# Kernel optimization log

Measured on AMD Instinct MI355X. Metric: run time of the kernel, lower is better.

## Reference

```python
import jax, jax.numpy as jnp
import numpy as np

B, N, C, H = 16384, 7, 512, 256  # batch, nodes(=n_classes), graph_hidden, hidden_layers
EPS = 1e-5


def bn(x, g, b):
    # training-mode BatchNorm1d over channels: stats over (batch, nodes)
    m = x.mean(axis=(0, 1))
    v = x.var(axis=(0, 1))  # biased variance, matches torch training BN
    return (x - m) * jax.lax.rsqrt(v + EPS) * g + b


def gcr(x, Wq, bq, Wk, bk, Wv, bv, gam):
    # GraphContextReasoning: SAGAN-style self-attention over the N node axis
    q = x @ Wq.T + bq            # [B, N, C/8]
    k = x @ Wk.T + bk            # [B, N, C/8]
    v = x @ Wv.T + bv            # [B, N, C]
    att = jax.nn.softmax(jnp.einsum('bnd,bmd->bnm', q, k), axis=-1)  # [B, N, N]
    return gam * jnp.einsum('bnm,bmc->bnc', att, v) + x


def setup_inputs() -> dict:
    ks = jax.random.split(jax.random.key(0), 40)
    it = iter(range(40))
    def rnd(shape, s=0.05):
        return jax.random.normal(ks[next(it)], shape, jnp.float32) * s
    d = {"x": jax.random.normal(ks[next(it)], (B, N, C), jnp.float32)}
    d["Wt"], d["bt"] = rnd((C, C)), rnd((C,))
    for i in ("1", "2", "3"):
        d["bn" + i + "_g"] = jnp.ones((C,), jnp.float32)
        d["bn" + i + "_b"] = jnp.zeros((C,), jnp.float32)
        d["Wq" + i], d["bq" + i] = rnd((C // 8, C)), rnd((C // 8,))
        d["Wk" + i], d["bk" + i] = rnd((C // 8, C)), rnd((C // 8,))
        d["Wv" + i], d["bv" + i] = rnd((C, C)), rnd((C,))
        d["gam" + i] = jnp.array(0.5, jnp.float32)  # torch inits 0; nonzero for nontrivial math
    d["Wb"], d["bb"] = rnd((H, C)), rnd((H,))
    return d


def reference(x, Wt, bt,
              bn1_g, bn1_b, Wq1, bq1, Wk1, bk1, Wv1, bv1, gam1,
              bn2_g, bn2_b, Wq2, bq2, Wk2, bk2, Wv2, bv2, gam2,
              bn3_g, bn3_b, Wq3, bq3, Wk3, bk3, Wv3, bv3, gam3,
              Wb, bb):
    # conv1x1 over channels == per-node linear; we keep (B, N, C) layout throughout
    h = x @ Wt.T + bt
    h = jax.nn.relu(gcr(bn(h, bn1_g, bn1_b), Wq1, bq1, Wk1, bk1, Wv1, bv1, gam1))
    h = jax.nn.relu(gcr(bn(h, bn2_g, bn2_b), Wq2, bq2, Wk2, bk2, Wv2, bv2, gam2))
    h = jax.nn.relu(gcr(bn(h, bn3_g, bn3_b), Wq3, bq3, Wk3, bk3, Wv3, bv3, gam3))
    return h @ Wb.T + bb  # [B, N, H]
```

## Files before the change

kernel.cpp:

```cpp
#include <hip/hip_runtime.h>
#include <hip/hip_bf16.h>
#include <stdint.h>


using bf16 = __hip_bfloat16;
typedef __attribute__((ext_vector_type(8))) short short8;
typedef __attribute__((ext_vector_type(4))) float f32x4;
typedef _Float16 f16x8 __attribute__((ext_vector_type(8)));

__device__ inline uint16_t f2b_bits(float f) {
  bf16 h = __float2bfloat16(f);
  return __builtin_bit_cast(uint16_t, h);
}
__device__ inline float b2f_bits(uint16_t u) { return __uint_as_float(((uint32_t)u) << 16); }
__device__ inline void split2(float v, uint16_t& hi, uint16_t& lo) {
  hi = f2b_bits(v);
  lo = f2b_bits(v - b2f_bits(hi));
}
__device__ inline uint16_t f2h_bits(float f) {
  _Float16 h = (_Float16)f;
  return __builtin_bit_cast(uint16_t, h);
}
__device__ inline float h2f_bits(uint16_t u) {
  return (float)__builtin_bit_cast(_Float16, u);
}
__device__ inline float g16(const uint4& u, int e) {
  uint32_t wrd = ((const uint32_t*)&u)[e >> 1];
  return h2f_bits((uint16_t)((e & 1) ? (wrd >> 16) : (wrd & 0xffffu)));
}

typedef const __attribute__((address_space(1))) void* gas_ptr;
typedef __attribute__((address_space(3))) void* las_ptr;
__device__ inline void gload16(const void* g, void* l) {
  __builtin_amdgcn_global_load_lds((gas_ptr)g, (las_ptr)l, 16, 0, 0);
}

__global__ __launch_bounds__(256) void cvt4h(const float* __restrict__ in,
                                             uint16_t* __restrict__ out, int n4) {
  int i = blockIdx.x * 256 + threadIdx.x;
  const int stride = gridDim.x * 256;
  for (; i < n4; i += stride) {
    float4 v = ((const float4*)in)[i];
    uint32_t lo = (uint32_t)f2h_bits(v.x) | ((uint32_t)f2h_bits(v.y) << 16);
    uint32_t hi = (uint32_t)f2h_bits(v.z) | ((uint32_t)f2h_bits(v.w) << 16);
    ((uint2*)out)[i] = make_uint2(lo, hi);
  }
}

__global__ __launch_bounds__(512) void fold_w_io(const float* __restrict__ Wsrc,
                                                 const float* __restrict__ bsrc,
                                                 char* __restrict__ Wio,
                                                 float* __restrict__ bout) {
  const int row = blockIdx.x, c = threadIdx.x;
  const float wv = Wsrc[(size_t)row * 512 + c];
  uint16_t hb, lb;
  split2(wv, hb, lb);
  char* p = Wio + (size_t)row * 2048 + (c >> 3) * 32 + (c & 7) * 2;
  *(uint16_t*)p = hb;
  *(uint16_t*)(p + 16) = lb;
  if (c == 0) bout[row] = bsrc[row];
}

__global__ __launch_bounds__(512) void fold_all(const float* __restrict__ Wq,
                                                const float* __restrict__ bq,
                                                const float* __restrict__ Wk,
                                                const float* __restrict__ bk,
                                                const float* __restrict__ Wv,
                                                const float* __restrict__ bv,
                                                const float* __restrict__ sv,
                                                const float* __restrict__ tv,
                                                const float* __restrict__ gamp,
                                                uint16_t* __restrict__ WqkH,
                                                uint16_t* __restrict__ WqkL,
                                                float* __restrict__ bqkf,
                                                uint16_t* __restrict__ WvH,
                                                float* __restrict__ bvf) {
  const int b = blockIdx.x, c = threadIdx.x;
  __shared__ float red[512];
  const float* Wsrc;
  const float* bsrc;
  uint16_t *Wh, *Wl;
  float* bout;
  float g;
  int row;
  if (b < 64) {
    Wsrc = Wq; bsrc = bq; Wh = WqkH; Wl = WqkL; bout = bqkf; g = 1.0f; row = b;
  } else if (b < 128) {
    Wsrc = Wk; bsrc = bk; Wh = WqkH + (size_t)64 * 512; Wl = WqkL + (size_t)64 * 512;
    bout = bqkf + 64; g = 1.0f; row = b - 64;
  } else {
    Wsrc = Wv; bsrc = bv; Wh = WvH; Wl = nullptr; bout = bvf; g = gamp[0]; row = b - 128;
  }
  const float wv = Wsrc[(size_t)row * 512 + c];
  const float fv = g * wv * sv[c];
  const uint16_t hb = f2h_bits(fv);
  Wh[(size_t)row * 512 + c] = hb;
  if (Wl) Wl[(size_t)row * 512 + c] = f2h_bits((fv - h2f_bits(hb)) * 1024.0f);
  red[c] = wv * tv[c];
  __syncthreads();
#pragma unroll
  for (int off = 256; off > 0; off >>= 1) {
    if (c < off) red[c] += red[c + off];
    __syncthreads();
  }
  if (c == 0) bout[row] = g * (bsrc[row] + red[0]);
}

__global__ __launch_bounds__(512, 1) void gemm1(const char* __restrict__ A,
                                                const char* __restrict__ Wio,
                                                const float* __restrict__ bias,
                                                uint16_t* __restrict__ outh,
                                                float* __restrict__ part) {
  constexpr int A_BYTES = 224 * 128;
  constexpr int PER_BUF = A_BYTES + 256 * 128;
  __shared__ __align__(16) char lds[2 * PER_BUF];
  __shared__ float sred[2][2][256];
  const int tid = threadIdx.x, w = tid >> 6, l = tid & 63;

  const int nwgx = gridDim.x;
  const int raw = blockIdx.y * nwgx + blockIdx.x;
  const int cpx = (nwgx * gridDim.y) >> 3;
  const int work = (raw & 7) * cpx + (raw >> 3);
  const int bmidx = work / nwgx;
  const int bm = bmidx * 224;
  const int bn = (work % nwgx) * 256;

  const int ssl = ((((l >> 1) & 3) ^ ((l >> 3) & 3)) << 5) | (((l & 1) ^ ((l >> 5) & 1)) << 4);
  const char* Asrc = A + (size_t)(bm + (l >> 3)) * 2048 + ssl;
  const char* Bsrc = Wio + (size_t)(bn + (l >> 3)) * 2048 + ssl;

  const int lrow = l & 15, lk = l >> 4;
  const int wr = w >> 2, wc = w & 3;
  const int sw32 = (lk ^ (lrow & 3)) * 32;
  const int hi16 = ((lrow >> 2) & 1) * 16;
  const int afr = (wr * 112 + lrow) * 128 + sw32;
  const int bfr = A_BYTES + (wc * 64 + lrow) * 128 + sw32;

  f32x4 acc[7][4] = {};

  auto stage_a = [&](int buf, int t) {
    char* dst = lds + buf * PER_BUF;
    const char* src = Asrc + (size_t)t * 128;
#pragma unroll
    for (int k = 0; k < 4; ++k) {
      const int i = w + k * 8;
      if (k < 3 || w < 4) gload16(src + (size_t)i * 16384, dst + i * 1024);
    }
  };
  auto stage_b = [&](int buf, int t) {
    char* dst = lds + buf * PER_BUF + A_BYTES;
    const char* src = Bsrc + (size_t)t * 128;
#pragma unroll
    for (int k = 0; k < 4; ++k) {
      const int i = w + k * 8;
      gload16(src + (size_t)i * 16384, dst + i * 1024);
    }
  };

#define LOADA(BASE, CNT)                                                         \
  {                                                                              \
    _Pragma("unroll") for (int u = 0; u < (CNT); ++u) {                          \
      const int mi = (BASE) + u;                                                 \
      float4 f0 = *(const float4*)(bp + afr + mi * 2048 + hi16);                 \
      float4 f1 = *(const float4*)(bp + afr + mi * 2048 + (hi16 ^ 16));          \
      const float fv[8] = {f0.x, f0.y, f0.z, f0.w, f1.x, f1.y, f1.z, f1.w};      \
      _Pragma("unroll") for (int e = 0; e < 8; ++e) {                            \
        uint16_t hb, lb;                                                         \
        split2(fv[e], hb, lb);                                                   \
        ah[u][e] = (short)hb;                                                    \
        al[u][e] = (short)lb;                                                    \
      }                                                                          \
    }                                                                            \
  }

#define MFMAC(BASE, CNT)                                                         \
  {                                                                              \
    __builtin_amdgcn_s_setprio(1);                                               \
    _Pragma("unroll") for (int u = 0; u < (CNT); ++u)                            \
      _Pragma("unroll") for (int ni = 0; ni < 4; ++ni)                           \
        acc[(BASE) + u][ni] = __builtin_amdgcn_mfma_f32_16x16x32_bf16(           \
            ah[u], bh[ni], acc[(BASE) + u][ni], 0, 0, 0);                        \
    _Pragma("unroll") for (int u = 0; u < (CNT); ++u)                            \
      _Pragma("unroll") for (int ni = 0; ni < 4; ++ni)                           \
        acc[(BASE) + u][ni] = __builtin_amdgcn_mfma_f32_16x16x32_bf16(           \
            ah[u], bl[ni], acc[(BASE) + u][ni], 0, 0, 0);                        \
    _Pragma("unroll") for (int u = 0; u < (CNT); ++u)                            \
      _Pragma("unroll") for (int ni = 0; ni < 4; ++ni)                           \
        acc[(BASE) + u][ni] = __builtin_amdgcn_mfma_f32_16x16x32_bf16(           \
            al[u], bh[ni], acc[(BASE) + u][ni], 0, 0, 0);                        \
    __builtin_amdgcn_s_setprio(0);                                               \
  }

  stage_a(0, 0);
  stage_b(0, 0);
  int cur = 0;
#pragma unroll 2
  for (int t = 0; t < 16; ++t) {
    asm volatile("s_waitcnt vmcnt(0)" ::: "memory");
    __builtin_amdgcn_s_barrier();
    asm volatile("" ::: "memory");

    const char* bp = lds + cur * PER_BUF;
    if (t < 15) stage_a(cur ^ 1, t + 1);

    short8 bh[4], bl[4];
#pragma unroll
    for (int ni = 0; ni < 4; ++ni) {
      bh[ni] = *(const short8*)(bp + bfr + ni * 2048 + hi16);
      bl[ni] = *(const short8*)(bp + bfr + ni * 2048 + (hi16 ^ 16));
    }
    short8 ah[4], al[4];
    LOADA(0, 4)
    MFMAC(0, 4)
    if (t < 15) stage_b(cur ^ 1, t + 1);
    LOADA(4, 3)
    MFMAC(4, 3)
    cur ^= 1;
  }
#undef LOADA
#undef MFMAC

  float sni[4] = {}, qni[4] = {};
#pragma unroll
  for (int mi = 0; mi < 7; ++mi) {
    const int row = bm + wr * 112 + mi * 16 + lk * 4;
#pragma unroll
    for (int ni = 0; ni < 4; ++ni) {
      const int col = bn + wc * 64 + ni * 16 + lrow;
      const float bc = bias[col];
#pragma unroll
      for (int j = 0; j < 4; ++j) {
        const float vv = acc[mi][ni][j] + bc;
        outh[(size_t)(row + j) * 512 + col] = f2h_bits(vv);
        sni[ni] += vv;
        qni[ni] += vv * vv;
      }
    }
  }
#pragma unroll
  for (int ni = 0; ni < 4; ++ni) {
    float s = sni[ni], q = qni[ni];
    s += __shfl_xor(s, 16); q += __shfl_xor(q, 16);
    s += __shfl_xor(s, 32); q += __shfl_xor(q, 32);
    if (lk == 0) {
      sred[0][wr][wc * 64 + ni * 16 + lrow] = s;
      sred[1][wr][wc * 64 + ni * 16 + lrow] = q;
    }
  }
  __syncthreads();
  if (tid < 256) {
    part[(size_t)bmidx * 1024 + bn + tid] = sred[0][0][tid] + sred[0][1][tid];
    part[(size_t)bmidx * 1024 + 512 + bn + tid] = sred[1][0][tid] + sred[1][1][tid];
  }
}

__global__ __launch_bounds__(512, 1) void sgemmV(const uint16_t* __restrict__ A,
                                                 const uint16_t* __restrict__ Wh,
                                                 const float* __restrict__ bias,
                                                 uint16_t* __restrict__ outh) {
  constexpr int A_BYTES = 112 * 128;
  constexpr int B_BYTES = 512 * 128;
  constexpr int PER_BUF = A_BYTES + B_BYTES;
  __shared__ __align__(16) char lds[2 * PER_BUF];
  const int tid = threadIdx.x, w = tid >> 6, l = tid & 63;

  const int raw = blockIdx.y;
  const int cpx = gridDim.y >> 3;
  const int bmidx = (raw & 7) * cpx + (raw >> 3);
  const int bm = bmidx * 112;

  const int sp = (((l & 7) ^ ((l >> 3) & 7)) << 4);
  const char* Asrc = (const char*)A + (size_t)(bm + (l >> 3)) * 1024 + sp;
  const char* Bhs = (const char*)Wh + (size_t)(l >> 3) * 1024 + sp;

  const int lrow = l & 15, lk = l >> 4;

  f32x4 acc[7][4] = {};

  auto stage_a = [&](int buf, int t) {
    char* dst = lds + buf * PER_BUF;
    const char* src = Asrc + t * 128;
#pragma unroll
    for (int k = 0; k < 2; ++k) {
      const int i = w + k * 8;
      if (k < 1 || w < 6) gload16(src + (size_t)i * 8192, dst + i * 1024);
    }
  };
  auto stage_b = [&](int buf, int t) {
    char* dst = lds + buf * PER_BUF + A_BYTES;
#pragma unroll
    for (int k = 0; k < 8; ++k) {
      const int i = w + k * 8;
      gload16(Bhs + t * 128 + (size_t)i * 8192, dst + i * 1024);
    }
  };

#define AFR(mi, kc) \
  (((mi)*16 + lrow) * 128 + ((((kc)*4 + lk) ^ (lrow & 7)) << 4))
#define BFR(ni, kc) \
  (A_BYTES + (w * 64 + (ni)*16 + lrow) * 128 + ((((kc)*4 + lk) ^ (lrow & 7)) << 4))

#define KHALF(kc)                                                                \
  {                                                                              \
    short8 bh[4];                                                                \
    _Pragma("unroll") for (int ni = 0; ni < 4; ++ni)                             \
        bh[ni] = *(const short8*)(bp + BFR(ni, kc));                             \
    short8 ah[7];                                                                \
    _Pragma("unroll") for (int mi = 0; mi < 7; ++mi)                             \
        ah[mi] = *(const short8*)(bp + AFR(mi, kc));                             \
    __builtin_amdgcn_s_setprio(1);                                               \
    _Pragma("unroll") for (int mi = 0; mi < 7; ++mi)                             \
      _Pragma("unroll") for (int ni = 0; ni < 4; ++ni)                           \
        acc[mi][ni] = __builtin_amdgcn_mfma_f32_16x16x32_f16(                    \
            __builtin_bit_cast(f16x8, ah[mi]), __builtin_bit_cast(f16x8, bh[ni]), \
            acc[mi][ni], 0, 0, 0);                                               \
    __builtin_amdgcn_s_setprio(0);                                               \
  }

  stage_a(0, 0);
  stage_b(0, 0);
  int cur = 0;
  for (int t = 0; t < 8; ++t) {
    asm volatile("s_waitcnt vmcnt(0)" ::: "memory");
    __builtin_amdgcn_s_barrier();
    asm volatile("" ::: "memory");
    const char* bp = lds + cur * PER_BUF;
    if (t < 7) stage_a(cur ^ 1, t + 1);
    KHALF(0)
    if (t < 7) stage_b(cur ^ 1, t + 1);
    KHALF(1)
    cur ^= 1;
  }
#undef KHALF
#undef AFR
#undef BFR

#pragma unroll
  for (int mi = 0; mi < 7; ++mi) {
    const int row = bm + mi * 16 + lk * 4;
#pragma unroll
    for (int ni = 0; ni < 4; ++ni) {
      const int col = w * 64 + ni * 16 + lrow;
      const float bc = bias[col];
#pragma unroll
      for (int j = 0; j < 4; ++j)
        outh[(size_t)(row + j) * 512 + col] = f2h_bits(acc[mi][ni][j] + bc);
    }
  }
}

__global__ __launch_bounds__(512, 1) void sgemm64(const uint16_t* __restrict__ A,
                                                  const uint16_t* __restrict__ Wh,
                                                  const float* __restrict__ bias,
                                                  float* __restrict__ outf, int N) {
  constexpr int BN = 256;
  constexpr int NFR = BN / 64;
  constexpr int A_BYTES = 224 * 128;
  constexpr int PER_BUF = A_BYTES + BN * 128;
  __shared__ __align__(16) char lds[2 * PER_BUF];
  const int tid = threadIdx.x, w = tid >> 6, l = tid & 63;

  const int nwgx = gridDim.x;
  const int raw = blockIdx.y * nwgx + blockIdx.x;
  const int cpx = (nwgx * gridDim.y) >> 3;
  const int work = (raw & 7) * cpx + (raw >> 3);
  const int bmidx = work / nwgx;
  const int bm = bmidx * 224;
  const int bn = (work % nwgx) * BN;

  const int sp = (((l & 7) ^ ((l >> 3) & 7)) << 4);
  const char* Asrc = (const char*)A + (size_t)(bm + (l >> 3)) * 1024 + sp;
  const char* Bhs = (const char*)Wh + (size_t)(bn + (l >> 3)) * 1024 + sp;

  const int lrow = l & 15, lk = l >> 4;
  const int wr = w >> 2, wc = w & 3;

  f32x4 acc[7][NFR] = {};

  auto stage_a = [&](int buf, int t) {
    char* dst = lds + buf * PER_BUF;
    const char* src = Asrc + t * 128;
#pragma unroll
    for (int k = 0; k < 4; ++k) {
      const int i = w + k * 8;
      if (k < 3 || w < 4) gload16(src + (size_t)i * 8192, dst + i * 1024);
    }
  };
  auto stage_b = [&](int buf, int t) {
    char* dst = lds + buf * PER_BUF + A_BYTES;
#pragma unroll
    for (int k = 0; k < BN / 64; ++k) {
      const int i = w + k * 8;
      gload16(Bhs + t * 128 + (size_t)i * 8192, dst + i * 1024);
    }
  };

#define AFR(mi, kc) \
  ((wr * 112 + (mi)*16 + lrow) * 128 + ((((kc)*4 + lk) ^ (lrow & 7)) << 4))
#define BFR(ni, kc) \
  (A_BYTES + (wc * (BN / 4) + (ni)*16 + lrow) * 128 + ((((kc)*4 + lk) ^ (lrow & 7)) << 4))

#define KHALF(kc)                                                                \
  {                                                                              \
    short8 bh[NFR];                                                              \
    _Pragma("unroll") for (int ni = 0; ni < NFR; ++ni)                           \
        bh[ni] = *(const short8*)(bp + BFR(ni, kc));                             \
    short8 ah[7];                                                                \
    _Pragma("unroll") for (int mi = 0; mi < 7; ++mi)                             \
        ah[mi] = *(const short8*)(bp + AFR(mi, kc));                             \
    __builtin_amdgcn_s_setprio(1);                                               \
    _Pragma("unroll") for (int mi = 0; mi < 7; ++mi)                             \
      _Pragma("unroll") for (int ni = 0; ni < NFR; ++ni)                         \
        acc[mi][ni] = __builtin_amdgcn_mfma_f32_16x16x32_f16(                    \
            __builtin_bit_cast(f16x8, ah[mi]), __builtin_bit_cast(f16x8, bh[ni]), \
            acc[mi][ni], 0, 0, 0);                                               \
    __builtin_amdgcn_s_setprio(0);                                               \
  }

  stage_a(0, 0);
  stage_b(0, 0);
  int cur = 0;
  for (int t = 0; t < 8; ++t) {
    asm volatile("s_waitcnt vmcnt(0)" ::: "memory");
    __builtin_amdgcn_s_barrier();
    asm volatile("" ::: "memory");
    const char* bp = lds + cur * PER_BUF;
    if (t < 7) stage_a(cur ^ 1, t + 1);
    KHALF(0)
    if (t < 7) stage_b(cur ^ 1, t + 1);
    KHALF(1)
    cur ^= 1;
  }
#undef KHALF
#undef AFR
#undef BFR

#pragma unroll
  for (int mi = 0; mi < 7; ++mi) {
    const int row = bm + wr * 112 + mi * 16 + lk * 4;
#pragma unroll
    for (int ni = 0; ni < NFR; ++ni) {
      const int col = bn + wc * (BN / 4) + ni * 16 + lrow;
      const float bc = bias[col];
#pragma unroll
      for (int j = 0; j < 4; ++j)
        outf[(size_t)(row + j) * N + col] = acc[mi][ni][j] + bc;
    }
  }
}

template <bool STATS>
__global__ __launch_bounds__(512, 1) void qkattn(const uint16_t* __restrict__ A,
                                                 const uint16_t* __restrict__ Wh,
                                                 const uint16_t* __restrict__ Wl,
                                                 const float* __restrict__ bias,
                                                 const uint16_t* __restrict__ V,
                                                 uint16_t* __restrict__ Hs,
                                                 const float* __restrict__ sv,
                                                 const float* __restrict__ tv,
                                                 float* __restrict__ part) {
  constexpr int A_BYTES = 224 * 128;
  constexpr int BPL = 128 * 128;
  constexpr int PER_BUF = A_BYTES + 2 * BPL;
  __shared__ __align__(16) char lds[131072];
  const int tid = threadIdx.x, w = tid >> 6, l = tid & 63;

  const int raw = blockIdx.y;
  const int cpx = gridDim.y >> 3;
  const int bmidx = (raw & 7) * cpx + (raw >> 3);
  const int bm = bmidx * 224;

  const int sp = (((l & 7) ^ ((l >> 3) & 7)) << 4);
  const char* Asrc = (const char*)A + (size_t)(bm + (l >> 3)) * 1024 + sp;
  const char* Bhs = (const char*)Wh + (size_t)(l >> 3) * 1024 + sp;
  const char* Bls = (const char*)Wl + (size_t)(l >> 3) * 1024 + sp;

  const int lrow = l & 15, lk = l >> 4;
  const int wr = w >> 2, wc = w & 3;

  f32x4 acc[7][2] = {};
  f32x4 acc2[7][2] = {};

  auto stage_a = [&](int buf, int t) {
    char* dst = lds + buf * PER_BUF;
    const char* src = Asrc + t * 128;
#pragma unroll
    for (int k = 0; k < 4; ++k) {
      const int i = w + k * 8;
      if (k < 3 || w < 4) gload16(src + (size_t)i * 8192, dst + i * 1024);
    }
  };
  auto stage_b = [&](int buf, int t) {
    char* dst = lds + buf * PER_BUF + A_BYTES;
#pragma unroll
    for (int k = 0; k < 2; ++k) {
      const int i = w + k * 8;
      gload16(Bhs + t * 128 + (size_t)i * 8192, dst + i * 1024);
      gload16(Bls + t * 128 + (size_t)i * 8192, dst + BPL + i * 1024);
    }
  };

#define AFR(mi, kc) \
  ((wr * 112 + (mi)*16 + lrow) * 128 + ((((kc)*4 + lk) ^ (lrow & 7)) << 4))
#define BFR(ni, kc) \
  (A_BYTES + (wc * 32 + (ni)*16 + lrow) * 128 + ((((kc)*4 + lk) ^ (lrow & 7)) << 4))

#define KHALF(kc)                                                                \
  {                                                                              \
    short8 bh[2], bl2[2];                                                        \
    _Pragma("unroll") for (int ni = 0; ni < 2; ++ni) {                           \
      bh[ni] = *(const short8*)(bp + BFR(ni, kc));                               \
      bl2[ni] = *(const short8*)(bp + BPL + BFR(ni, kc));                        \
    }                                                                            \
    short8 ah[7];                                                                \
    _Pragma("unroll") for (int mi = 0; mi < 7; ++mi)                             \
        ah[mi] = *(const short8*)(bp + AFR(mi, kc));                             \
    __builtin_amdgcn_s_setprio(1);                                               \
    _Pragma("unroll") for (int mi = 0; mi < 7; ++mi)                             \
      _Pragma("unroll") for (int ni = 0; ni < 2; ++ni)                           \
        acc[mi][ni] = __builtin_amdgcn_mfma_f32_16x16x32_f16(                    \
            __builtin_bit_cast(f16x8, ah[mi]), __builtin_bit_cast(f16x8, bh[ni]), \
            acc[mi][ni], 0, 0, 0);                                               \
    _Pragma("unroll") for (int mi = 0; mi < 7; ++mi)                             \
      _Pragma("unroll") for (int ni = 0; ni < 2; ++ni)                           \
        acc2[mi][ni] = __builtin_amdgcn_mfma_f32_16x16x32_f16(                   \
            __builtin_bit_cast(f16x8, ah[mi]), __builtin_bit_cast(f16x8, bl2[ni]), \
            acc2[mi][ni], 0, 0, 0);                                              \
    __builtin_amdgcn_s_setprio(0);                                               \
  }

  stage_a(0, 0);
  stage_b(0, 0);
  int cur = 0;
  for (int t = 0; t < 8; ++t) {
    asm volatile("s_waitcnt vmcnt(0)" ::: "memory");
    __builtin_amdgcn_s_barrier();
    asm volatile("" ::: "memory");
    const char* bp = lds + cur * PER_BUF;
    if (t < 7) stage_a(cur ^ 1, t + 1);
    KHALF(0)
    if (t < 7) stage_b(cur ^ 1, t + 1);
    KHALF(1)
    cur ^= 1;
  }
#undef KHALF
#undef AFR
#undef BFR

  __syncthreads();
  float* qk = (float*)lds;
#pragma unroll
  for (int mi = 0; mi < 7; ++mi) {
    const int rl = wr * 112 + mi * 16 + lk * 4;
#pragma unroll
    for (int ni = 0; ni < 2; ++ni) {
      const int col = wc * 32 + ni * 16 + lrow;
      const float bc = bias[col];
#pragma unroll
      for (int j = 0; j < 4; ++j)
        qk[(rl + j) * 128 + col] = acc[mi][ni][j] + bc + acc2[mi][ni][j] * (1.0f / 1024.0f);
    }
  }
  __syncthreads();

  const float4 s0 = *(const float4*)&sv[l * 8], s1 = *(const float4*)&sv[l * 8 + 4];
  const float4 t0 = *(const float4*)&tv[l * 8], t1 = *(const float4*)&tv[l * 8 + 4];
  const float sarr[8] = {s0.x, s0.y, s0.z, s0.w, s1.x, s1.y, s1.z, s1.w};
  const float tarr[8] = {t0.x, t0.y, t0.z, t0.w, t1.x, t1.y, t1.z, t1.w};

  float s8[8] = {}, q8[8] = {};
#pragma unroll
  for (int gg = 0; gg < 4; ++gg) {
    const int g = w * 4 + gg;
    const int rl = g * 7;
    const size_t base = (size_t)bm + rl;

    float qv[7], kv[7];
#pragma unroll
    for (int i = 0; i < 7; ++i) {
      qv[i] = qk[(rl + i) * 128 + l];
      kv[i] = qk[(rl + i) * 128 + 64 + l];
    }
    float att[7][7];
#pragma unroll
    for (int i = 0; i < 7; ++i)
#pragma unroll
      for (int j = 0; j < 7; ++j) {
        float p = qv[i] * kv[j];
#pragma unroll
        for (int o = 32; o; o >>= 1) p += __shfl_xor(p, o);
        att[i][j] = p;
      }
#pragma unroll
    for (int i = 0; i < 7; ++i) {
      float m = att[i][0];
#pragma unroll
      for (int j = 1; j < 7; ++j) m = fmaxf(m, att[i][j]);
      float sum = 0.f;
#pragma unroll
      for (int j = 0; j < 7; ++j) {
        att[i][j] = expf(att[i][j] - m);
        sum += att[i][j];
      }
      const float inv = 1.0f / sum;
#pragma unroll
      for (int j = 0; j < 7; ++j) att[i][j] *= inv;
    }

    uint4 vpk[7];
#pragma unroll
    for (int j = 0; j < 7; ++j)
      vpk[j] = *(const uint4*)((const char*)V + (base + j) * 1024 + l * 16);

#pragma unroll
    for (int i = 0; i < 7; ++i) {
      char* hp = (char*)Hs + (base + i) * 1024 + l * 16;
      uint4 hh = *(const uint4*)hp;
      float o[8] = {};
#pragma unroll
      for (int j = 0; j < 7; ++j) {
        const float a = att[i][j];
#pragma unroll
        for (int e = 0; e < 8; ++e) o[e] += a * g16(vpk[j], e);
      }
      uint16_t oh[8];
#pragma unroll
      for (int e = 0; e < 8; ++e) {
        const float xn = g16(hh, e) * sarr[e] + tarr[e];
        const float rr = fmaxf(o[e] + xn, 0.f);
        if constexpr (STATS) { s8[e] += rr; q8[e] += rr * rr; }
        oh[e] = f2h_bits(rr);
      }
      uint4 ph;
#pragma unroll
      for (int k2 = 0; k2 < 4; ++k2)
        ((uint32_t*)&ph)[k2] = (uint32_t)oh[2 * k2] | ((uint32_t)oh[2 * k2 + 1] << 16);
      *(uint4*)hp = ph;
    }
  }

  if constexpr (STATS) {
    float* sred = (float*)(lds + 114688);
#pragma unroll
    for (int e = 0; e < 8; ++e) sred[w * 512 + l * 8 + e] = s8[e];
    __syncthreads();
    {
      float sum = 0.f;
#pragma unroll
      for (int ww = 0; ww < 8; ++ww) sum += sred[ww * 512 + tid];
      part[(size_t)bmidx * 1024 + tid] = sum;
    }
    __syncthreads();
#pragma unroll
    for (int e = 0; e < 8; ++e) sred[w * 512 + l * 8 + e] = q8[e];
    __syncthreads();
    {
      float sum = 0.f;
#pragma unroll
      for (int ww = 0; ww < 8; ++ww) sum += sred[ww * 512 + tid];
      part[(size_t)bmidx * 1024 + 512 + tid] = sum;
    }
  }
}

__global__ __launch_bounds__(64) void reduce_stats(const float* __restrict__ part, int n,
                                                   const float* __restrict__ g,
                                                   const float* __restrict__ bb,
                                                   float* __restrict__ sv,
                                                   float* __restrict__ tv) {
  const int c = blockIdx.x, k = threadIdx.x;
  float sum = 0.f, sq = 0.f;
  for (int i = k; i < n; i += 64) {
    const float* p = part + (size_t)i * 1024;
    sum += p[c];
    sq += p[512 + c];
  }
#pragma unroll
  for (int o = 32; o; o >>= 1) {
    sum += __shfl_xor(sum, o);
    sq += __shfl_xor(sq, o);
  }
  if (k == 0) {
    const float mean = sum * (1.0f / 114688.0f);
    const float var = sq * (1.0f / 114688.0f) - mean * mean;
    const float sc = g[c] * rsqrtf(var + 1e-5f);
    sv[c] = sc;
    tv[c] = bb[c] - mean * sc;
  }
}

extern "C" void kernel_launch(void* const* d_in, const int* in_sizes, int n_in,
                              void* d_out, int out_size, void* d_ws, size_t ws_size,
                              hipStream_t stream) {
  const float* x  = (const float*)d_in[0];
  const float* Wt = (const float*)d_in[1];
  const float* bt = (const float*)d_in[2];
  const float *bng[3], *bnb[3], *Wq[3], *bq[3], *Wk[3], *bk[3], *Wv[3], *bv[3], *gam[3];
  for (int i = 0; i < 3; ++i) {
    int o = 3 + 9 * i;
    bng[i] = (const float*)d_in[o + 0];
    bnb[i] = (const float*)d_in[o + 1];
    Wq[i]  = (const float*)d_in[o + 2];
    bq[i]  = (const float*)d_in[o + 3];
    Wk[i]  = (const float*)d_in[o + 4];
    bk[i]  = (const float*)d_in[o + 5];
    Wv[i]  = (const float*)d_in[o + 6];
    bv[i]  = (const float*)d_in[o + 7];
    gam[i] = (const float*)d_in[o + 8];
  }
  const float* Wb = (const float*)d_in[30];
  const float* bb = (const float*)d_in[31];

  char* ws = (char*)d_ws;
  uint16_t* Hs    = (uint16_t*)(ws);
  uint16_t* V     = (uint16_t*)(ws + 117440512);
  float*    part  = (float*)(ws + 234881024);
  float*    sv    = (float*)(ws + 236978176);
  float*    tv    = (float*)(ws + 236980224);
  uint16_t* WqkH  = (uint16_t*)(ws + 236982272);
  uint16_t* WqkL  = (uint16_t*)(ws + 237113344);
  float*    bqkf  = (float*)(ws + 237244416);
  uint16_t* WvH   = (uint16_t*)(ws + 237246464);
  float*    bvf   = (float*)(ws + 237770752);
  char*     WtIo  = ws + 237772800;
  float*    btf   = (float*)(ws + 238821376);
  uint16_t* WbH   = (uint16_t*)(ws + 238823424);

  cvt4h<<<128, 256, 0, stream>>>(Wb, WbH, 32768);
  fold_w_io<<<512, 512, 0, stream>>>(Wt, bt, WtIo, btf);

  gemm1<<<dim3(2, 512), 512, 0, stream>>>((const char*)x, WtIo, btf, Hs, part);

  for (int i = 0; i < 3; ++i) {
    reduce_stats<<<512, 64, 0, stream>>>(part, 512, bng[i], bnb[i], sv, tv);
    fold_all<<<640, 512, 0, stream>>>(Wq[i], bq[i], Wk[i], bk[i], Wv[i], bv[i],
                                      sv, tv, gam[i], WqkH, WqkL, bqkf, WvH, bvf);
    sgemmV<<<dim3(1, 1024), 512, 0, stream>>>(Hs, WvH, bvf, V);
    if (i < 2)
      qkattn<true><<<dim3(1, 512), 512, 0, stream>>>(Hs, WqkH, WqkL, bqkf, V, Hs,
                                                     sv, tv, part);
    else
      qkattn<false><<<dim3(1, 512), 512, 0, stream>>>(Hs, WqkH, WqkL, bqkf, V, Hs,
                                                      sv, tv, nullptr);
  }

  sgemm64<<<dim3(1, 512), 512, 0, stream>>>(Hs, WbH, bb, (float*)d_out, 256);
}
```

Before: 946.0 us.

## Fuse V projection into attention kernel and stage Q/K through fp16 buffer

The fusion boundary moves: the V GEMM now runs inside the attention kernel, and its result stays in LDS instead of making an fp16 round trip through global memory. Q/K is now computed in a separate GEMM kernel that writes fp16 values into the output buffer, which serves as scratch. The attention kernel reads them back from there. Stats partials are now produced by 1024 blocks instead of 512, and the reduce count is adjusted for that. The trade is a large V write/read removed for a much smaller Q/K round trip, plus lower Q/K precision (fp16 storage).

```diff
diff --git a/kernel.cpp b/kernel.cpp
--- a/kernel.cpp
+++ b/kernel.cpp
@@ -254,215 +254,15 @@
   }
 }
 
-__global__ __launch_bounds__(512, 1) void sgemmV(const uint16_t* __restrict__ A,
-                                                 const uint16_t* __restrict__ Wh,
-                                                 const float* __restrict__ bias,
-                                                 uint16_t* __restrict__ outh) {
-  constexpr int A_BYTES = 112 * 128;
-  constexpr int B_BYTES = 512 * 128;
-  constexpr int PER_BUF = A_BYTES + B_BYTES;
-  __shared__ __align__(16) char lds[2 * PER_BUF];
-  const int tid = threadIdx.x, w = tid >> 6, l = tid & 63;
-
-  const int raw = blockIdx.y;
-  const int cpx = gridDim.y >> 3;
-  const int bmidx = (raw & 7) * cpx + (raw >> 3);
-  const int bm = bmidx * 112;
-
-  const int sp = (((l & 7) ^ ((l >> 3) & 7)) << 4);
-  const char* Asrc = (const char*)A + (size_t)(bm + (l >> 3)) * 1024 + sp;
-  const char* Bhs = (const char*)Wh + (size_t)(l >> 3) * 1024 + sp;
-
-  const int lrow = l & 15, lk = l >> 4;
-
-  f32x4 acc[7][4] = {};
-
-  auto stage_a = [&](int buf, int t) {
-    char* dst = lds + buf * PER_BUF;
-    const char* src = Asrc + t * 128;
-#pragma unroll
-    for (int k = 0; k < 2; ++k) {
-      const int i = w + k * 8;
-      if (k < 1 || w < 6) gload16(src + (size_t)i * 8192, dst + i * 1024);
-    }
-  };
-  auto stage_b = [&](int buf, int t) {
-    char* dst = lds + buf * PER_BUF + A_BYTES;
-#pragma unroll
-    for (int k = 0; k < 8; ++k) {
-      const int i = w + k * 8;
-      gload16(Bhs + t * 128 + (size_t)i * 8192, dst + i * 1024);
-    }
-  };
-
-#define AFR(mi, kc) \
-  (((mi)*16 + lrow) * 128 + ((((kc)*4 + lk) ^ (lrow & 7)) << 4))
-#define BFR(ni, kc) \
-  (A_BYTES + (w * 64 + (ni)*16 + lrow) * 128 + ((((kc)*4 + lk) ^ (lrow & 7)) << 4))
-
-#define KHALF(kc)                                                                \
-  {                                                                              \
-    short8 bh[4];                                                                \
-    _Pragma("unroll") for (int ni = 0; ni < 4; ++ni)                             \
-        bh[ni] = *(const short8*)(bp + BFR(ni, kc));                             \
-    short8 ah[7];                                                                \
-    _Pragma("unroll") for (int mi = 0; mi < 7; ++mi)                             \
-        ah[mi] = *(const short8*)(bp + AFR(mi, kc));                             \
-    __builtin_amdgcn_s_setprio(1);                                               \
-    _Pragma("unroll") for (int mi = 0; mi < 7; ++mi)                             \
-      _Pragma("unroll") for (int ni = 0; ni < 4; ++ni)                           \
-        acc[mi][ni] = __builtin_amdgcn_mfma_f32_16x16x32_f16(                    \
-            __builtin_bit_cast(f16x8, ah[mi]), __builtin_bit_cast(f16x8, bh[ni]), \
-            acc[mi][ni], 0, 0, 0);                                               \
-    __builtin_amdgcn_s_setprio(0);                                               \
-  }
-
-  stage_a(0, 0);
-  stage_b(0, 0);
-  int cur = 0;
-  for (int t = 0; t < 8; ++t) {
-    asm volatile("s_waitcnt vmcnt(0)" ::: "memory");
-    __builtin_amdgcn_s_barrier();
-    asm volatile("" ::: "memory");
-    const char* bp = lds + cur * PER_BUF;
-    if (t < 7) stage_a(cur ^ 1, t + 1);
-    KHALF(0)
-    if (t < 7) stage_b(cur ^ 1, t + 1);
-    KHALF(1)
-    cur ^= 1;
-  }
-#undef KHALF
-#undef AFR
-#undef BFR
-
-#pragma unroll
-  for (int mi = 0; mi < 7; ++mi) {
-    const int row = bm + mi * 16 + lk * 4;
-#pragma unroll
-    for (int ni = 0; ni < 4; ++ni) {
-      const int col = w * 64 + ni * 16 + lrow;
-      const float bc = bias[col];
-#pragma unroll
-      for (int j = 0; j < 4; ++j)
-        outh[(size_t)(row + j) * 512 + col] = f2h_bits(acc[mi][ni][j] + bc);
-    }
-  }
-}
-
-__global__ __launch_bounds__(512, 1) void sgemm64(const uint16_t* __restrict__ A,
-                                                  const uint16_t* __restrict__ Wh,
-                                                  const float* __restrict__ bias,
-                                                  float* __restrict__ outf, int N) {
-  constexpr int BN = 256;
-  constexpr int NFR = BN / 64;
-  constexpr int A_BYTES = 224 * 128;
-  constexpr int PER_BUF = A_BYTES + BN * 128;
-  __shared__ __align__(16) char lds[2 * PER_BUF];
-  const int tid = threadIdx.x, w = tid >> 6, l = tid & 63;
-
-  const int nwgx = gridDim.x;
-  const int raw = blockIdx.y * nwgx + blockIdx.x;
-  const int cpx = (nwgx * gridDim.y) >> 3;
-  const int work = (raw & 7) * cpx + (raw >> 3);
-  const int bmidx = work / nwgx;
-  const int bm = bmidx * 224;
-  const int bn = (work % nwgx) * BN;
-
-  const int sp = (((l & 7) ^ ((l >> 3) & 7)) << 4);
-  const char* Asrc = (const char*)A + (size_t)(bm + (l >> 3)) * 1024 + sp;
-  const char* Bhs = (const char*)Wh + (size_t)(bn + (l >> 3)) * 1024 + sp;
-
-  const int lrow = l & 15, lk = l >> 4;
-  const int wr = w >> 2, wc = w & 3;
-
-  f32x4 acc[7][NFR] = {};
-
-  auto stage_a = [&](int buf, int t) {
-    char* dst = lds + buf * PER_BUF;
-    const char* src = Asrc + t * 128;
-#pragma unroll
-    for (int k = 0; k < 4; ++k) {
-      const int i = w + k * 8;
-      if (k < 3 || w < 4) gload16(src + (size_t)i * 8192, dst + i * 1024);
-    }
-  };
-  auto stage_b = [&](int buf, int t) {
-    char* dst = lds + buf * PER_BUF + A_BYTES;
-#pragma unroll
-    for (int k = 0; k < BN / 64; ++k) {
-      const int i = w + k * 8;
-      gload16(Bhs + t * 128 + (size_t)i * 8192, dst + i * 1024);
-    }
-  };
-
-#define AFR(mi, kc) \
-  ((wr * 112 + (mi)*16 + lrow) * 128 + ((((kc)*4 + lk) ^ (lrow & 7)) << 4))
-#define BFR(ni, kc) \
-  (A_BYTES + (wc * (BN / 4) + (ni)*16 + lrow) * 128 + ((((kc)*4 + lk) ^ (lrow & 7)) << 4))
-
-#define KHALF(kc)                                                                \
-  {                                                                              \
-    short8 bh[NFR];                                                              \
-    _Pragma("unroll") for (int ni = 0; ni < NFR; ++ni)                           \
-        bh[ni] = *(const short8*)(bp + BFR(ni, kc));                             \
-    short8 ah[7];                                                                \
-    _Pragma("unroll") for (int mi = 0; mi < 7; ++mi)                             \
-        ah[mi] = *(const short8*)(bp + AFR(mi, kc));                             \
-    __builtin_amdgcn_s_setprio(1);                                               \
-    _Pragma("unroll") for (int mi = 0; mi < 7; ++mi)                             \
-      _Pragma("unroll") for (int ni = 0; ni < NFR; ++ni)                         \
-        acc[mi][ni] = __builtin_amdgcn_mfma_f32_16x16x32_f16(                    \
-            __builtin_bit_cast(f16x8, ah[mi]), __builtin_bit_cast(f16x8, bh[ni]), \
-            acc[mi][ni], 0, 0, 0);                                               \
-    __builtin_amdgcn_s_setprio(0);                                               \
-  }
-
-  stage_a(0, 0);
-  stage_b(0, 0);
-  int cur = 0;
-  for (int t = 0; t < 8; ++t) {
-    asm volatile("s_waitcnt vmcnt(0)" ::: "memory");
-    __builtin_amdgcn_s_barrier();
-    asm volatile("" ::: "memory");
-    const char* bp = lds + cur * PER_BUF;
-    if (t < 7) stage_a(cur ^ 1, t + 1);
-    KHALF(0)
-    if (t < 7) stage_b(cur ^ 1, t + 1);
-    KHALF(1)
-    cur ^= 1;
-  }
-#undef KHALF
-#undef AFR
-#undef BFR
-
-#pragma unroll
-  for (int mi = 0; mi < 7; ++mi) {
-    const int row = bm + wr * 112 + mi * 16 + lk * 4;
-#pragma unroll
-    for (int ni = 0; ni < NFR; ++ni) {
-      const int col = bn + wc * (BN / 4) + ni * 16 + lrow;
-      const float bc = bias[col];
-#pragma unroll
-      for (int j = 0; j < 4; ++j)
-        outf[(size_t)(row + j) * N + col] = acc[mi][ni][j] + bc;
-    }
-  }
-}
-
-template <bool STATS>
-__global__ __launch_bounds__(512, 1) void qkattn(const uint16_t* __restrict__ A,
+__global__ __launch_bounds__(512, 1) void qkgemm(const uint16_t* __restrict__ A,
                                                  const uint16_t* __restrict__ Wh,
                                                  const uint16_t* __restrict__ Wl,
                                                  const float* __restrict__ bias,
-                                                 const uint16_t* __restrict__ V,
-                                                 uint16_t* __restrict__ Hs,
-                                                 const float* __restrict__ sv,
-                                                 const float* __restrict__ tv,
-                                                 float* __restrict__ part) {
+                                                 uint16_t* __restrict__ qkh) {
   constexpr int A_BYTES = 224 * 128;
   constexpr int BPL = 128 * 128;
   constexpr int PER_BUF = A_BYTES + 2 * BPL;
-  __shared__ __align__(16) char lds[131072];
+  __shared__ __align__(16) char lds[2 * PER_BUF];
   const int tid = threadIdx.x, w = tid >> 6, l = tid & 63;
 
   const int raw = blockIdx.y;
@@ -547,19 +347,123 @@
 #undef AFR
 #undef BFR
 
-  __syncthreads();
-  float* qk = (float*)lds;
 #pragma unroll
   for (int mi = 0; mi < 7; ++mi) {
-    const int rl = wr * 112 + mi * 16 + lk * 4;
+    const int row = bm + wr * 112 + mi * 16 + lk * 4;
 #pragma unroll
     for (int ni = 0; ni < 2; ++ni) {
       const int col = wc * 32 + ni * 16 + lrow;
       const float bc = bias[col];
 #pragma unroll
       for (int j = 0; j < 4; ++j)
-        qk[(rl + j) * 128 + col] = acc[mi][ni][j] + bc + acc2[mi][ni][j] * (1.0f / 1024.0f);
-    }
+        qkh[(size_t)(row + j) * 128 + col] =
+            f2h_bits(acc[mi][ni][j] + bc + acc2[mi][ni][j] * (1.0f / 1024.0f));
+    }
+  }
+}
+
+template <bool STATS>
+__global__ __launch_bounds__(512, 1) void vattn(const uint16_t* __restrict__ A,
+                                                const uint16_t* __restrict__ Wh,
+                                                const float* __restrict__ bias,
+                                                const uint16_t* __restrict__ qkh,
+                                                uint16_t* __restrict__ Hs,
+                                                const float* __restrict__ sv,
+                                                const float* __restrict__ tv,
+                                                float* __restrict__ part) {
+  constexpr int A_BYTES = 112 * 128;
+  constexpr int B_BYTES = 512 * 128;
+  constexpr int PER_BUF = A_BYTES + B_BYTES;
+  __shared__ __align__(16) char lds[2 * PER_BUF];
+  const int tid = threadIdx.x, w = tid >> 6, l = tid & 63;
+
+  const int raw = blockIdx.y;
+  const int cpx = gridDim.y >> 3;
+  const int bmidx = (raw & 7) * cpx + (raw >> 3);
+  const int bm = bmidx * 112;
+
+  const int sp = (((l & 7) ^ ((l >> 3) & 7)) << 4);
+  const char* Asrc = (const char*)A + (size_t)(bm + (l >> 3)) * 1024 + sp;
+  const char* Bhs = (const char*)Wh + (size_t)(l >> 3) * 1024 + sp;
+
+  const int lrow = l & 15, lk = l >> 4;
+
+  f32x4 acc[7][4] = {};
+
+  auto stage_a = [&](int buf, int t) {
+    char* dst = lds + buf * PER_BUF;
+    const char* src = Asrc + t * 128;
+#pragma unroll
+    for (int k = 0; k < 2; ++k) {
+      const int i = w + k * 8;
+      if (k < 1 || w < 6) gload16(src + (size_t)i * 8192, dst + i * 1024);
+    }
+  };
+  auto stage_b = [&](int buf, int t) {
+    char* dst = lds + buf * PER_BUF + A_BYTES;
+#pragma unroll
+    for (int k = 0; k < 8; ++k) {
+      const int i = w + k * 8;
+      gload16(Bhs + t * 128 + (size_t)i * 8192, dst + i * 1024);
+    }
+  };
+
+#define AFR(mi, kc) \
+  (((mi)*16 + lrow) * 128 + ((((kc)*4 + lk) ^ (lrow & 7)) << 4))
+#define BFR(ni, kc) \
+  (A_BYTES + (w * 64 + (ni)*16 + lrow) * 128 + ((((kc)*4 + lk) ^ (lrow & 7)) << 4))
+
+#define KHALF(kc)                                                                \
+  {                                                                              \
+    short8 bh[4];                                                                \
+    _Pragma("unroll") for (int ni = 0; ni < 4; ++ni)                             \
+        bh[ni] = *(const short8*)(bp + BFR(ni, kc));                             \
+    short8 ah[7];                                                                \
+    _Pragma("unroll") for (int mi = 0; mi < 7; ++mi)                             \
+        ah[mi] = *(const short8*)(bp + AFR(mi, kc));                             \
+    __builtin_amdgcn_s_setprio(1);                                               \
+    _Pragma("unroll") for (int mi = 0; mi < 7; ++mi)                             \
+      _Pragma("unroll") for (int ni = 0; ni < 4; ++ni)                           \
+        acc[mi][ni] = __builtin_amdgcn_mfma_f32_16x16x32_f16(                    \
+            __builtin_bit_cast(f16x8, ah[mi]), __builtin_bit_cast(f16x8, bh[ni]), \
+            acc[mi][ni], 0, 0, 0);                                               \
+    __builtin_amdgcn_s_setprio(0);                                               \
+  }
+
+  stage_a(0, 0);
+  stage_b(0, 0);
+  int cur = 0;
+  for (int t = 0; t < 8; ++t) {
+    asm volatile("s_waitcnt vmcnt(0)" ::: "memory");
+    __builtin_amdgcn_s_barrier();
+    asm volatile("" ::: "memory");
+    const char* bp = lds + cur * PER_BUF;
+    if (t < 7) stage_a(cur ^ 1, t + 1);
+    KHALF(0)
+    if (t < 7) stage_b(cur ^ 1, t + 1);
+    KHALF(1)
+    cur ^= 1;
+  }
+#undef KHALF
+#undef AFR
+#undef BFR
+
+  __syncthreads();
+  {
+    uint16_t* vl = (uint16_t*)lds;
+#pragma unroll
+    for (int mi = 0; mi < 7; ++mi)
+#pragma unroll
+      for (int ni = 0; ni < 4; ++ni) {
+        const int col = w * 64 + ni * 16 + lrow;
+        const float bc = bias[col];
+#pragma unroll
+        for (int j = 0; j < 4; ++j) {
+          const int row = mi * 16 + lk * 4 + j;
+          const int g = row / 7, jj = row - g * 7;
+          vl[g * 4096 + jj * 512 + col] = f2h_bits(acc[mi][ni][j] + bc);
+        }
+      }
   }
   __syncthreads();
 
@@ -570,16 +474,15 @@
 
   float s8[8] = {}, q8[8] = {};
 #pragma unroll
-  for (int gg = 0; gg < 4; ++gg) {
-    const int g = w * 4 + gg;
-    const int rl = g * 7;
-    const size_t base = (size_t)bm + rl;
+  for (int gg = 0; gg < 2; ++gg) {
+    const int g = w * 2 + gg;
+    const size_t grow = (size_t)bm + g * 7;
 
     float qv[7], kv[7];
 #pragma unroll
     for (int i = 0; i < 7; ++i) {
-      qv[i] = qk[(rl + i) * 128 + l];
-      kv[i] = qk[(rl + i) * 128 + 64 + l];
+      qv[i] = h2f_bits(qkh[(grow + i) * 128 + l]);
+      kv[i] = h2f_bits(qkh[(grow + i) * 128 + 64 + l]);
     }
     float att[7][7];
 #pragma unroll
@@ -610,11 +513,11 @@
     uint4 vpk[7];
 #pragma unroll
     for (int j = 0; j < 7; ++j)
-      vpk[j] = *(const uint4*)((const char*)V + (base + j) * 1024 + l * 16);
+      vpk[j] = *(const uint4*)(lds + g * 8192 + j * 1024 + l * 16);
 
 #pragma unroll
     for (int i = 0; i < 7; ++i) {
-      char* hp = (char*)Hs + (base + i) * 1024 + l * 16;
+      char* hp = (char*)Hs + (grow + i) * 1024 + l * 16;
       uint4 hh = *(const uint4*)hp;
       float o[8] = {};
 #pragma unroll
@@ -640,7 +543,8 @@
   }
 
   if constexpr (STATS) {
-    float* sred = (float*)(lds + 114688);
+    __syncthreads();
+    float* sred = (float*)lds;
 #pragma unroll
     for (int e = 0; e < 8; ++e) sred[w * 512 + l * 8 + e] = s8[e];
     __syncthreads();
@@ -659,6 +563,104 @@
 #pragma unroll
       for (int ww = 0; ww < 8; ++ww) sum += sred[ww * 512 + tid];
       part[(size_t)bmidx * 1024 + 512 + tid] = sum;
+    }
+  }
+}
+
+__global__ __launch_bounds__(512, 1) void sgemm64(const uint16_t* __restrict__ A,
+                                                  const uint16_t* __restrict__ Wh,
+                                                  const float* __restrict__ bias,
+                                                  float* __restrict__ outf, int N) {
+  constexpr int BN = 256;
+  constexpr int NFR = BN / 64;
+  constexpr int A_BYTES = 224 * 128;
+  constexpr int PER_BUF = A_BYTES + BN * 128;
+  __shared__ __align__(16) char lds[2 * PER_BUF];
+  const int tid = threadIdx.x, w = tid >> 6, l = tid & 63;
+
+  const int raw = blockIdx.y;
+  const int cpx = gridDim.y >> 3;
+  const int bmidx = (raw & 7) * cpx + (raw >> 3);
+  const int bm = bmidx * 224;
+  const int bn = 0;
+
+  const int sp = (((l & 7) ^ ((l >> 3) & 7)) << 4);
+  const char* Asrc = (const char*)A + (size_t)(bm + (l >> 3)) * 1024 + sp;
+  const char* Bhs = (const char*)Wh + (size_t)(bn + (l >> 3)) * 1024 + sp;
+
+  const int lrow = l & 15, lk = l >> 4;
+  const int wr = w >> 2, wc = w & 3;
+
+  f32x4 acc[7][NFR] = {};
+
+  auto stage_a = [&](int buf, int t) {
+    char* dst = lds + buf * PER_BUF;
+    const char* src = Asrc + t * 128;
+#pragma unroll
+    for (int k = 0; k < 4; ++k) {
+      const int i = w + k * 8;
+      if (k < 3 || w < 4) gload16(src + (size_t)i * 8192, dst + i * 1024);
+    }
+  };
+  auto stage_b = [&](int buf, int t) {
+    char* dst = lds + buf * PER_BUF + A_BYTES;
+#pragma unroll
+    for (int k = 0; k < BN / 64; ++k) {
+      const int i = w + k * 8;
+      gload16(Bhs + t * 128 + (size_t)i * 8192, dst + i * 1024);
+    }
+  };
+
+#define AFR(mi, kc) \
+  ((wr * 112 + (mi)*16 + lrow) * 128 + ((((kc)*4 + lk) ^ (lrow & 7)) << 4))
+#define BFR(ni, kc) \
+  (A_BYTES + (wc * (BN / 4) + (ni)*16 + lrow) * 128 + ((((kc)*4 + lk) ^ (lrow & 7)) << 4))
+
+#define KHALF(kc)                                                                \
+  {                                                                              \
+    short8 bh[NFR];                                                              \
+    _Pragma("unroll") for (int ni = 0; ni < NFR; ++ni)                           \
+        bh[ni] = *(const short8*)(bp + BFR(ni, kc));                             \
+    short8 ah[7];                                                                \
+    _Pragma("unroll") for (int mi = 0; mi < 7; ++mi)                             \
+        ah[mi] = *(const short8*)(bp + AFR(mi, kc));                             \
+    __builtin_amdgcn_s_setprio(1);                                               \
+    _Pragma("unroll") for (int mi = 0; mi < 7; ++mi)                             \
+      _Pragma("unroll") for (int ni = 0; ni < NFR; ++ni)                         \
+        acc[mi][ni] = __builtin_amdgcn_mfma_f32_16x16x32_f16(                    \
+            __builtin_bit_cast(f16x8, ah[mi]), __builtin_bit_cast(f16x8, bh[ni]), \
+            acc[mi][ni], 0, 0, 0);                                               \
+    __builtin_amdgcn_s_setprio(0);                                               \
+  }
+
+  stage_a(0, 0);
+  stage_b(0, 0);
+  int cur = 0;
+  for (int t = 0; t < 8; ++t) {
+    asm volatile("s_waitcnt vmcnt(0)" ::: "memory");
+    __builtin_amdgcn_s_barrier();
+    asm volatile("" ::: "memory");
+    const char* bp = lds + cur * PER_BUF;
+    if (t < 7) stage_a(cur ^ 1, t + 1);
+    KHALF(0)
+    if (t < 7) stage_b(cur ^ 1, t + 1);
+    KHALF(1)
+    cur ^= 1;
+  }
+#undef KHALF
+#undef AFR
+#undef BFR
+
+#pragma unroll
+  for (int mi = 0; mi < 7; ++mi) {
+    const int row = bm + wr * 112 + mi * 16 + lk * 4;
+#pragma unroll
+    for (int ni = 0; ni < NFR; ++ni) {
+      const int col = bn + wc * (BN / 4) + ni * 16 + lrow;
+      const float bc = bias[col];
+#pragma unroll
+      for (int j = 0; j < 4; ++j)
+        outf[(size_t)(row + j) * N + col] = acc[mi][ni][j] + bc;
     }
   }
 }
@@ -713,18 +715,18 @@
 
   char* ws = (char*)d_ws;
   uint16_t* Hs    = (uint16_t*)(ws);
-  uint16_t* V     = (uint16_t*)(ws + 117440512);
-  float*    part  = (float*)(ws + 234881024);
-  float*    sv    = (float*)(ws + 236978176);
-  float*    tv    = (float*)(ws + 236980224);
-  uint16_t* WqkH  = (uint16_t*)(ws + 236982272);
-  uint16_t* WqkL  = (uint16_t*)(ws + 237113344);
-  float*    bqkf  = (float*)(ws + 237244416);
-  uint16_t* WvH   = (uint16_t*)(ws + 237246464);
-  float*    bvf   = (float*)(ws + 237770752);
-  char*     WtIo  = ws + 237772800;
-  float*    btf   = (float*)(ws + 238821376);
-  uint16_t* WbH   = (uint16_t*)(ws + 238823424);
+  float*    part  = (float*)(ws + 117440512);
+  float*    sv    = (float*)(ws + 121634816);
+  float*    tv    = (float*)(ws + 121636864);
+  uint16_t* WqkH  = (uint16_t*)(ws + 121638912);
+  uint16_t* WqkL  = (uint16_t*)(ws + 121769984);
+  float*    bqkf  = (float*)(ws + 121901056);
+  uint16_t* WvH   = (uint16_t*)(ws + 121903104);
+  float*    bvf   = (float*)(ws + 122427392);
+  char*     WtIo  = ws + 122429440;
+  float*    btf   = (float*)(ws + 123478016);
+  uint16_t* WbH   = (uint16_t*)(ws + 123480064);
+  uint16_t* qkh   = (uint16_t*)d_out;
 
   cvt4h<<<128, 256, 0, stream>>>(Wb, WbH, 32768);
   fold_w_io<<<512, 512, 0, stream>>>(Wt, bt, WtIo, btf);
@@ -732,15 +734,16 @@
   gemm1<<<dim3(2, 512), 512, 0, stream>>>((const char*)x, WtIo, btf, Hs, part);
 
   for (int i = 0; i < 3; ++i) {
-    reduce_stats<<<512, 64, 0, stream>>>(part, 512, bng[i], bnb[i], sv, tv);
+    reduce_stats<<<512, 64, 0, stream>>>(part, i == 0 ? 512 : 1024,
+                                         bng[i], bnb[i], sv, tv);
     fold_all<<<640, 512, 0, stream>>>(Wq[i], bq[i], Wk[i], bk[i], Wv[i], bv[i],
                                       sv, tv, gam[i], WqkH, WqkL, bqkf, WvH, bvf);
-    sgemmV<<<dim3(1, 1024), 512, 0, stream>>>(Hs, WvH, bvf, V);
+    qkgemm<<<dim3(1, 512), 512, 0, stream>>>(Hs, WqkH, WqkL, bqkf, qkh);
     if (i < 2)
-      qkattn<true><<<dim3(1, 512), 512, 0, stream>>>(Hs, WqkH, WqkL, bqkf, V, Hs,
+      vattn<true><<<dim3(1, 1024), 512, 0, stream>>>(Hs, WvH, bvf, qkh, Hs,
                                                      sv, tv, part);
     else
-      qkattn<false><<<dim3(1, 512), 512, 0, stream>>>(Hs, WqkH, WqkL, bqkf, V, Hs,
+      vattn<false><<<dim3(1, 1024), 512, 0, stream>>>(Hs, WvH, bvf, qkh, Hs,
                                                       sv, tv, nullptr);
   }
 
```

After: 915.8 us. 3.2% less time.
